# Kernel optimization log

Hardware: AMD Instinct MI355X
Metric: run time of the kernel (lower is better)

Reference implementation:

```python
import jax, jax.numpy as jnp
import numpy as np

D = 128  # d_pair
N = 512  # n_res
B = 1
EPS = 1e-5


def setup_inputs() -> dict:
    key = jax.random.key(0)
    ks = jax.random.split(key, 16)
    s = 0.02
    inp = {
        "pair": jax.random.normal(ks[0], (B, N, N, D), dtype=jnp.float32),
        "pair_mask": jnp.ones((B, N, N), dtype=jnp.float32),
        "ln_g": jnp.ones((D,), dtype=jnp.float32),
        "ln_b": jnp.zeros((D,), dtype=jnp.float32),
        "w_lp": jax.random.normal(ks[1], (D, D), dtype=jnp.float32) * s,
        "b_lp": jnp.zeros((D,), dtype=jnp.float32),
        "w_lg": jax.random.normal(ks[2], (D, D), dtype=jnp.float32) * s,
        "b_lg": jnp.zeros((D,), dtype=jnp.float32),
        "w_rp": jax.random.normal(ks[3], (D, D), dtype=jnp.float32) * s,
        "b_rp": jnp.zeros((D,), dtype=jnp.float32),
        "w_rg": jax.random.normal(ks[4], (D, D), dtype=jnp.float32) * s,
        "b_rg": jnp.zeros((D,), dtype=jnp.float32),
        "w_g": jax.random.normal(ks[5], (D, D), dtype=jnp.float32) * s,
        "b_g": jnp.zeros((D,), dtype=jnp.float32),
        "w_o": jax.random.normal(ks[6], (D, D), dtype=jnp.float32) * s,
        "b_o": jnp.zeros((D,), dtype=jnp.float32),
    }
    return inp


def _layer_norm(x, g, b):
    mu = jnp.mean(x, axis=-1, keepdims=True)
    var = jnp.mean(jnp.square(x - mu), axis=-1, keepdims=True)
    return (x - mu) * jax.lax.rsqrt(var + EPS) * g + b


def reference(pair, pair_mask, ln_g, ln_b, w_lp, b_lp, w_lg, b_lg,
              w_rp, b_rp, w_rg, b_rg, w_g, b_g, w_o, b_o):
    # [B,N,N,D] pair representation; outgoing triangle multiplication
    x = _layer_norm(pair, ln_g, ln_b)
    mask = pair_mask[..., None]  # [B,N,N,1]
    left = (x @ w_lp + b_lp) * jax.nn.sigmoid(x @ w_lg + b_lg) * mask
    right = (x @ w_rp + b_rp) * jax.nn.sigmoid(x @ w_rg + b_rg) * mask
    # outgoing: contract over j -> per-channel NxN matmul
    out = jnp.einsum('bijd,bjkd->bikd', left, right)
    out = out * jax.nn.sigmoid(x @ w_g + b_g)
    out = out @ w_o + b_o
    return out
```

## Files before the change

kernel.cpp:

```cpp
#include <hip/hip_runtime.h>

#define NN 512
#define DD 128
#define PP (NN*NN)

typedef __attribute__((ext_vector_type(8))) short short8;
typedef __attribute__((ext_vector_type(4))) float floatx4;
typedef __attribute__((ext_vector_type(4))) unsigned int uintx4;
typedef __attribute__((ext_vector_type(2))) unsigned int uintx2;

__device__ __forceinline__ unsigned short f2bf(float f) {
  unsigned int u = __float_as_uint(f);
  u += 0x7fffu + ((u >> 16) & 1u);
  return (unsigned short)(u >> 16);
}
__device__ __forceinline__ float bf2f(unsigned short h) {
  return __uint_as_float(((unsigned int)h) << 16);
}
__device__ __forceinline__ unsigned int pkbf2(float lo, float hi) {
  unsigned int r;
  asm("v_cvt_pk_bf16_f32 %0, %1, %2" : "=v"(r) : "v"(lo), "v"(hi));
  return r;
}
__device__ __forceinline__ float sigm(float x) {
  return 1.f / (1.f + __expf(-x));
}

__device__ __forceinline__ void gload_lds16(const unsigned short* g, unsigned short* l) {
  __builtin_amdgcn_global_load_lds(
      (const __attribute__((address_space(1))) unsigned int*)g,
      (__attribute__((address_space(3))) unsigned int*)l, 16, 0, 0);
}

__global__ void k0_prep(const float* __restrict__ wlp, const float* __restrict__ wlg,
                        const float* __restrict__ wrp, const float* __restrict__ wrg,
                        const float* __restrict__ wg,  const float* __restrict__ wo,
                        unsigned short* __restrict__ wt) {
  const float* src[6] = {wlp, wlg, wrp, wrg, wg, wo};
  int m = blockIdx.y;
  int idx = blockIdx.x * 256 + threadIdx.x;
  int d = idx >> 7, e = idx & 127;
  wt[m * 16384 + e * 128 + d] = f2bf(src[m][d * 128 + e]);
}

__launch_bounds__(256, 8)
__global__ void k1a_ln(const float* __restrict__ pair,
                       const float* __restrict__ lng, const float* __restrict__ lnb,
                       unsigned short* __restrict__ xln) {
  const int t = threadIdx.x;
  const int sub = t & 31;
  const long row0 = (long)blockIdx.x * 128 + (t >> 5);
  const floatx4 g4 = *(const floatx4*)(lng + sub * 4);
  const floatx4 b4 = *(const floatx4*)(lnb + sub * 4);
  const float* src = pair + row0 * DD + sub * 4;
  unsigned short* dst = xln + row0 * DD + sub * 4;
  floatx4 vn = *(const floatx4*)src;
  #pragma unroll
  for (int pass = 0; pass < 16; ++pass) {
    floatx4 v = vn;
    if (pass < 15) vn = *(const floatx4*)(src + (pass + 1) * 8 * DD);
    float s  = v.x + v.y + v.z + v.w;
    float s2 = v.x * v.x + v.y * v.y + v.z * v.z + v.w * v.w;
    #pragma unroll
    for (int m = 1; m < 32; m <<= 1) {
      s  += __shfl_xor(s, m);
      s2 += __shfl_xor(s2, m);
    }
    float mu = s * (1.f / 128.f);
    float rs = rsqrtf(s2 * (1.f / 128.f) - mu * mu + 1e-5f);
    uintx2 o;
    o[0] = pkbf2((v.x - mu) * rs * g4.x + b4.x, (v.y - mu) * rs * g4.y + b4.y);
    o[1] = pkbf2((v.z - mu) * rs * g4.z + b4.z, (v.w - mu) * rs * g4.w + b4.w);
    *(uintx2*)(dst + pass * 8 * DD) = o;
  }
}

__launch_bounds__(512, 4)
__global__ void k1b_proj(const unsigned short* __restrict__ xln,
                         const float* __restrict__ pmask,
                         const unsigned short* __restrict__ wt,
                         const float* __restrict__ b_lp, const float* __restrict__ b_lg,
                         const float* __restrict__ b_rp, const float* __restrict__ b_rg,
                         const float* __restrict__ b_g,
                         unsigned short* __restrict__ left_t,
                         unsigned short* __restrict__ right_bt,
                         unsigned short* __restrict__ gate_t) {
  __shared__ __align__(16) unsigned short Sm[24576];
  __shared__ float Mlds[128];

  const int t = threadIdx.x;
  const int unit = blockIdx.y;
  const int q = blockIdx.x;

  int j0 = 0, kk = 0;
  long p0 = 0, soff;
  if (unit == 1) {
    j0 = (q >> 9) << 7; kk = q & 511;
    soff = (long)kk * NN + j0;
  } else {
    p0 = (long)q << 7;
    soff = p0;
  }
  auto arow = [&](int r) -> long {
    return (unit == 1) ? ((long)(j0 + r) * NN + kk) : (p0 + r);
  };

  if (unit < 2 && t < 128) Mlds[t] = pmask[arow(t)];

  const unsigned short* wA = wt + (unit == 0 ? 0 : unit == 1 ? 2 : 4) * 16384;
  const unsigned short* wB = wt + (unit == 0 ? 1 : 3) * 16384;

  const int lane = t & 63, w = t >> 6;
  const int ln = lane & 15, q8 = lane >> 4;
  const int wm = (w >> 2) << 6, we = (w & 3) << 5;
  const int sr = t >> 2, sc = t & 3;

  const long aBase = arow(sr) * DD + sc * 8;

  auto STAGE = [&](int set, int kc) {
    unsigned short* base = Sm + set * 12288;
    gload_lds16(xln + aBase + kc * 32,            &base[t * 8]);
    gload_lds16(wA + sr * 128 + kc * 32 + sc * 8, &base[4096 + t * 8]);
    if (unit < 2)
      gload_lds16(wB + sr * 128 + kc * 32 + sc * 8, &base[8192 + t * 8]);
  };

  floatx4 aP[4][2] = {}, aG[4][2] = {};
  STAGE(0, 0);
  __syncthreads();
  #pragma unroll
  for (int kc = 0; kc < 4; ++kc) {
    const int cur = kc & 1;
    if (kc < 3) STAGE(cur ^ 1, kc + 1);
    unsigned short* Al = Sm + cur * 12288;
    unsigned short* Bp = Al + 4096;
    unsigned short* Bg = Al + 8192;
    short8 a[4];
    #pragma unroll
    for (int i = 0; i < 4; ++i)
      a[i] = *(const short8*)&Al[(wm + i * 16 + ln) * 32 + q8 * 8];
    #pragma unroll
    for (int j = 0; j < 2; ++j) {
      short8 bpv = *(const short8*)&Bp[(we + j * 16 + ln) * 32 + q8 * 8];
      #pragma unroll
      for (int i = 0; i < 4; ++i)
        aP[i][j] = __builtin_amdgcn_mfma_f32_16x16x32_bf16(a[i], bpv, aP[i][j], 0, 0, 0);
    }
    if (unit < 2) {
      #pragma unroll
      for (int j = 0; j < 2; ++j) {
        short8 bgv = *(const short8*)&Bg[(we + j * 16 + ln) * 32 + q8 * 8];
        #pragma unroll
        for (int i = 0; i < 4; ++i)
          aG[i][j] = __builtin_amdgcn_mfma_f32_16x16x32_bf16(a[i], bgv, aG[i][j], 0, 0, 0);
      }
    }
    __syncthreads();
  }

  unsigned short* mystg = Sm + w * 2176;
  if (unit < 2) {
    const float* bpp = (unit == 0) ? b_lp : b_rp;
    const float* bgg = (unit == 0) ? b_lg : b_rg;
    #pragma unroll
    for (int j = 0; j < 2; ++j) {
      int eg = we + j * 16 + ln;
      float bp = bpp[eg], bg = bgg[eg];
      #pragma unroll
      for (int i = 0; i < 4; ++i) {
        float vv[4];
        #pragma unroll
        for (int r = 0; r < 4; ++r) {
          int m = wm + i * 16 + q8 * 4 + r;
          vv[r] = (aP[i][j][r] + bp) * sigm(aG[i][j][r] + bg) * Mlds[m];
        }
        unsigned int* du = (unsigned int*)&mystg[(j * 16 + ln) * 68 + i * 16 + q8 * 4];
        du[0] = pkbf2(vv[0], vv[1]);
        du[1] = pkbf2(vv[2], vv[3]);
      }
    }
  } else {
    #pragma unroll
    for (int j = 0; j < 2; ++j) {
      int eg = we + j * 16 + ln;
      float bg = b_g[eg];
      #pragma unroll
      for (int i = 0; i < 4; ++i) {
        float vv[4];
        #pragma unroll
        for (int r = 0; r < 4; ++r)
          vv[r] = sigm(aP[i][j][r] + bg);
        unsigned int* du = (unsigned int*)&mystg[(j * 16 + ln) * 68 + i * 16 + q8 * 4];
        du[0] = pkbf2(vv[0], vv[1]);
        du[1] = pkbf2(vv[2], vv[3]);
      }
    }
  }

  unsigned short* dstbase = (unit == 0) ? left_t : (unit == 1 ? right_bt : gate_t);
  #pragma unroll
  for (int itr = 0; itr < 4; ++itr) {
    int row = itr * 8 + (lane >> 3);
    int c = lane & 7;
    short8 vv = *(const short8*)&mystg[row * 68 + c * 8];
    long eg = we + row;
    *(short8*)(dstbase + eg * PP + soff + wm + c * 8) = vv;
  }
}

__launch_bounds__(512, 4)
__global__ void k2_einsum(const unsigned short* __restrict__ left_t,
                          const unsigned short* __restrict__ right_bt,
                          const unsigned short* __restrict__ gate_t,
                          unsigned short* __restrict__ tmpg) {
  __shared__ __align__(16) unsigned short Sm[16896];
  unsigned short* Cl = Sm;
  const int t = threadIdx.x;
  const int h = blockIdx.x;
  const int L = (h & 7) * 256 + (h >> 3);
  const int d = L >> 4;
  const int tile = L & 15;
  const int i0 = (tile >> 2) << 7;
  const int k0 = (tile & 3) << 7;
  const unsigned short* Ag = left_t   + (long)d * PP;
  const unsigned short* Bg = right_bt + (long)d * PP;
  const unsigned short* Gg = gate_t   + (long)d * PP;
  const int lane = t & 63, w = t >> 6;
  const int ln = lane & 15, q8 = lane >> 4;
  const int wm = (w >> 2) << 6, wn = (w & 3) << 5;
  const int sr = t >> 2, sc = t & 3;

  const long aBase = (long)(i0 + sr) * NN + sc * 8;
  const long bBase = (long)(k0 + sr) * NN + sc * 8;

  auto STAGE = [&](int set, int jj) {
    gload_lds16(Ag + aBase + jj, &Sm[set * 8192 + t * 8]);
    gload_lds16(Bg + bBase + jj, &Sm[set * 8192 + 4096 + t * 8]);
  };

  floatx4 acc[4][2] = {};
  STAGE(0, 0);
  __syncthreads();
  for (int it = 0; it < 16; ++it) {
    const int cur = it & 1;
    if (it < 15) STAGE(cur ^ 1, (it + 1) * 32);
    unsigned short* Al = Sm + cur * 8192;
    unsigned short* Bl = Al + 4096;
    short8 a[4], b[2];
    #pragma unroll
    for (int i = 0; i < 4; ++i)
      a[i] = *(const short8*)&Al[(wm + i * 16 + ln) * 32 + q8 * 8];
    #pragma unroll
    for (int j = 0; j < 2; ++j)
      b[j] = *(const short8*)&Bl[(wn + j * 16 + ln) * 32 + q8 * 8];
    #pragma unroll
    for (int i = 0; i < 4; ++i)
      #pragma unroll
      for (int j = 0; j < 2; ++j)
        acc[i][j] = __builtin_amdgcn_mfma_f32_16x16x32_bf16(a[i], b[j], acc[i][j], 0, 0, 0);
    __syncthreads();
  }
  #pragma unroll
  for (int i = 0; i < 4; ++i)
    #pragma unroll
    for (int j = 0; j < 2; ++j) {
      int n = wn + j * 16 + ln;
      #pragma unroll
      for (int r = 0; r < 4; ++r) {
        int m = wm + i * 16 + q8 * 4 + r;
        float gf = bf2f(Gg[(long)(i0 + m) * NN + k0 + n]);
        Cl[m * 132 + n] = f2bf(acc[i][j][r] * gf);
      }
    }
  __syncthreads();
  unsigned short* Og = tmpg + (long)d * PP;
  #pragma unroll
  for (int it = 0; it < 4; ++it) {
    int flat = it * 512 + t;
    int m = flat >> 4, c = flat & 15;
    *(short8*)(Og + (long)(i0 + m) * NN + k0 + c * 8) = *(const short8*)&Cl[m * 132 + c * 8];
  }
}

__launch_bounds__(512, 4)
__global__ void k3_out(const unsigned short* __restrict__ tmpg,
                       const unsigned short* __restrict__ wt,
                       const float* __restrict__ b_o,
                       float* __restrict__ out) {
  __shared__ __align__(16) unsigned short Tl[128 * 144];
  unsigned int* TlU = (unsigned int*)Tl;
  const int t = threadIdx.x;
  const long p0 = (long)blockIdx.x << 7;
  const unsigned short* wo = wt + 5 * 16384;

  #pragma unroll
  for (int it = 0; it < 2; ++it) {
    int flat = it * 512 + t;
    int rp = flat >> 4;
    int c  = flat & 15;
    const unsigned short* ra = tmpg + (long)(2 * rp) * PP + p0 + c * 8;
    uintx4 xa = *(const uintx4*)ra;
    uintx4 xb = *(const uintx4*)(ra + PP);
    int sw = ((c & 7) << 3) ^ ((c >> 3) << 2);
    #pragma unroll
    for (int cc = 0; cc < 4; ++cc) {
      int p = c * 8 + 2 * cc;
      TlU[p * 72 + (rp ^ sw)]       = (xa[cc] & 0xffffu) | (xb[cc] << 16);
      TlU[(p + 1) * 72 + (rp ^ sw)] = (xa[cc] >> 16) | (xb[cc] & 0xffff0000u);
    }
  }
  __syncthreads();

  const int lane = t & 63, w = t >> 6;
  const int ln = lane & 15, q8 = lane >> 4;
  const int wm = (w >> 2) << 6, wn = (w & 3) << 5;

  floatx4 acc[4][2] = {};
  #pragma unroll
  for (int ks = 0; ks < 4; ++ks) {
    short8 a[4], b[2];
    #pragma unroll
    for (int i = 0; i < 4; ++i) {
      int p = wm + i * 16 + ln;
      int swh = (((p >> 3) & 7) << 4) ^ (((p >> 6) & 1) << 3);
      a[i] = *(const short8*)&Tl[p * 144 + ((ks * 32 + q8 * 8) ^ swh)];
    }
    #pragma unroll
    for (int j = 0; j < 2; ++j)
      b[j] = *(const short8*)(wo + (wn + j * 16 + ln) * 128 + ks * 32 + q8 * 8);
    #pragma unroll
    for (int i = 0; i < 4; ++i)
      #pragma unroll
      for (int j = 0; j < 2; ++j)
        acc[i][j] = __builtin_amdgcn_mfma_f32_16x16x32_bf16(a[i], b[j], acc[i][j], 0, 0, 0);
  }
  #pragma unroll
  for (int j = 0; j < 2; ++j) {
    int eg = wn + j * 16 + ln;
    float bias = b_o[eg];
    #pragma unroll
    for (int i = 0; i < 4; ++i)
      #pragma unroll
      for (int r = 0; r < 4; ++r) {
        int m = wm + i * 16 + q8 * 4 + r;
        out[(p0 + m) * DD + eg] = acc[i][j][r] + bias;
      }
  }
}

extern "C" void kernel_launch(void* const* d_in, const int* in_sizes, int n_in,
                              void* d_out, int out_size, void* d_ws, size_t ws_size,
                              hipStream_t stream) {
  const float* pair = (const float*)d_in[0];
  const float* pmask = (const float*)d_in[1];
  const float* ln_g = (const float*)d_in[2];
  const float* ln_b = (const float*)d_in[3];
  const float* w_lp = (const float*)d_in[4];
  const float* b_lp = (const float*)d_in[5];
  const float* w_lg = (const float*)d_in[6];
  const float* b_lg = (const float*)d_in[7];
  const float* w_rp = (const float*)d_in[8];
  const float* b_rp = (const float*)d_in[9];
  const float* w_rg = (const float*)d_in[10];
  const float* b_rg = (const float*)d_in[11];
  const float* w_g  = (const float*)d_in[12];
  const float* b_g  = (const float*)d_in[13];
  const float* w_o  = (const float*)d_in[14];
  const float* b_o  = (const float*)d_in[15];
  float* out = (float*)d_out;

  char* ws = (char*)d_ws;
  unsigned short* wt       = (unsigned short*)ws;
  unsigned short* xln      = (unsigned short*)(ws + 196608);
  unsigned short* left_t   = xln      + (size_t)PP * DD;
  unsigned short* right_bt = left_t   + (size_t)PP * DD;
  unsigned short* gate_t   = right_bt + (size_t)PP * DD;
  unsigned short* tmpg     = xln;

  k0_prep<<<dim3(64, 6), 256, 0, stream>>>(w_lp, w_lg, w_rp, w_rg, w_g, w_o, wt);
  k1a_ln<<<dim3(2048), 256, 0, stream>>>(pair, ln_g, ln_b, xln);
  k1b_proj<<<dim3(2048, 3), 512, 0, stream>>>(xln, pmask, wt,
      b_lp, b_lg, b_rp, b_rg, b_g, left_t, right_bt, gate_t);
  k2_einsum<<<dim3(2048), 512, 0, stream>>>(left_t, right_bt, gate_t, tmpg);
  k3_out<<<dim3(2048), 512, 0, stream>>>(tmpg, wt, b_o, out);
}
```

Baseline: 477.1 us.

## Split projection kernel so left and gate share one staged xln tile

The single three-unit projection kernel becomes two kernels. One computes both the gate and the left projections from one 128-row xln tile kept in LDS across all four k-chunks. The other computes the right projection with its transposed row access. This removes one of the three global reads of the xln tile per row block. In exchange the combined kernel uses more LDS (about 70KB), which may lower occupancy, and its weight loads are no longer double-buffered, so loads and MFMA work overlap less.

Result: slower. 491.2 us (+3.0%).

```diff
diff --git a/kernel.cpp b/kernel.cpp
--- a/kernel.cpp
+++ b/kernel.cpp
@@ -76,53 +76,169 @@
 }
 
 __launch_bounds__(512, 4)
-__global__ void k1b_proj(const unsigned short* __restrict__ xln,
-                         const float* __restrict__ pmask,
-                         const unsigned short* __restrict__ wt,
-                         const float* __restrict__ b_lp, const float* __restrict__ b_lg,
-                         const float* __restrict__ b_rp, const float* __restrict__ b_rg,
-                         const float* __restrict__ b_g,
-                         unsigned short* __restrict__ left_t,
-                         unsigned short* __restrict__ right_bt,
-                         unsigned short* __restrict__ gate_t) {
-  __shared__ __align__(16) unsigned short Sm[24576];
+__global__ void k1b_lg(const unsigned short* __restrict__ xln,
+                       const float* __restrict__ pmask,
+                       const unsigned short* __restrict__ wt,
+                       const float* __restrict__ b_lp, const float* __restrict__ b_lg,
+                       const float* __restrict__ b_g,
+                       unsigned short* __restrict__ left_t,
+                       unsigned short* __restrict__ gate_t) {
+  __shared__ __align__(16) unsigned short Sm[34816];
   __shared__ float Mlds[128];
+  unsigned short* Areg = Sm;
+  unsigned short* Wreg = Sm + 17408;
 
   const int t = threadIdx.x;
-  const int unit = blockIdx.y;
-  const int q = blockIdx.x;
-
-  int j0 = 0, kk = 0;
-  long p0 = 0, soff;
-  if (unit == 1) {
-    j0 = (q >> 9) << 7; kk = q & 511;
-    soff = (long)kk * NN + j0;
-  } else {
-    p0 = (long)q << 7;
-    soff = p0;
-  }
-  auto arow = [&](int r) -> long {
-    return (unit == 1) ? ((long)(j0 + r) * NN + kk) : (p0 + r);
-  };
-
-  if (unit < 2 && t < 128) Mlds[t] = pmask[arow(t)];
-
-  const unsigned short* wA = wt + (unit == 0 ? 0 : unit == 1 ? 2 : 4) * 16384;
-  const unsigned short* wB = wt + (unit == 0 ? 1 : 3) * 16384;
+  const long p0 = (long)blockIdx.x << 7;
+  if (t < 128) Mlds[t] = pmask[p0 + t];
 
   const int lane = t & 63, w = t >> 6;
   const int ln = lane & 15, q8 = lane >> 4;
   const int wm = (w >> 2) << 6, we = (w & 3) << 5;
   const int sr = t >> 2, sc = t & 3;
 
+  const unsigned short* wlp = wt;
+  const unsigned short* wlg = wt + 16384;
+  const unsigned short* wg  = wt + 4 * 16384;
+
+  #pragma unroll
+  for (int kc = 0; kc < 4; ++kc)
+    gload_lds16(xln + (p0 + sr) * DD + kc * 32 + sc * 8, &Areg[kc * 4096 + t * 8]);
+
+  floatx4 aG2[4][2] = {};
+  #pragma unroll
+  for (int kc = 0; kc < 4; ++kc) {
+    gload_lds16(wg + sr * 128 + kc * 32 + sc * 8, &Wreg[t * 8]);
+    __syncthreads();
+    short8 a[4];
+    #pragma unroll
+    for (int i = 0; i < 4; ++i)
+      a[i] = *(const short8*)&Areg[kc * 4096 + (wm + i * 16 + ln) * 32 + q8 * 8];
+    #pragma unroll
+    for (int j = 0; j < 2; ++j) {
+      short8 bv = *(const short8*)&Wreg[(we + j * 16 + ln) * 32 + q8 * 8];
+      #pragma unroll
+      for (int i = 0; i < 4; ++i)
+        aG2[i][j] = __builtin_amdgcn_mfma_f32_16x16x32_bf16(a[i], bv, aG2[i][j], 0, 0, 0);
+    }
+    __syncthreads();
+  }
+  {
+    unsigned short* stg = Wreg + w * 2176;
+    #pragma unroll
+    for (int j = 0; j < 2; ++j) {
+      int eg = we + j * 16 + ln;
+      float bg = b_g[eg];
+      #pragma unroll
+      for (int i = 0; i < 4; ++i) {
+        float vv[4];
+        #pragma unroll
+        for (int r = 0; r < 4; ++r)
+          vv[r] = sigm(aG2[i][j][r] + bg);
+        unsigned int* du = (unsigned int*)&stg[(j * 16 + ln) * 68 + i * 16 + q8 * 4];
+        du[0] = pkbf2(vv[0], vv[1]);
+        du[1] = pkbf2(vv[2], vv[3]);
+      }
+    }
+    #pragma unroll
+    for (int itr = 0; itr < 4; ++itr) {
+      int row = itr * 8 + (lane >> 3);
+      int c = lane & 7;
+      short8 vv = *(const short8*)&stg[row * 68 + c * 8];
+      long eg = we + row;
+      *(short8*)(gate_t + eg * PP + p0 + wm + c * 8) = vv;
+    }
+  }
+  __syncthreads();
+
+  floatx4 aP[4][2] = {}, aG[4][2] = {};
+  #pragma unroll
+  for (int kc = 0; kc < 4; ++kc) {
+    gload_lds16(wlp + sr * 128 + kc * 32 + sc * 8, &Wreg[t * 8]);
+    gload_lds16(wlg + sr * 128 + kc * 32 + sc * 8, &Wreg[4096 + t * 8]);
+    __syncthreads();
+    short8 a[4];
+    #pragma unroll
+    for (int i = 0; i < 4; ++i)
+      a[i] = *(const short8*)&Areg[kc * 4096 + (wm + i * 16 + ln) * 32 + q8 * 8];
+    #pragma unroll
+    for (int j = 0; j < 2; ++j) {
+      short8 bpv = *(const short8*)&Wreg[(we + j * 16 + ln) * 32 + q8 * 8];
+      #pragma unroll
+      for (int i = 0; i < 4; ++i)
+        aP[i][j] = __builtin_amdgcn_mfma_f32_16x16x32_bf16(a[i], bpv, aP[i][j], 0, 0, 0);
+    }
+    #pragma unroll
+    for (int j = 0; j < 2; ++j) {
+      short8 bgv = *(const short8*)&Wreg[4096 + (we + j * 16 + ln) * 32 + q8 * 8];
+      #pragma unroll
+      for (int i = 0; i < 4; ++i)
+        aG[i][j] = __builtin_amdgcn_mfma_f32_16x16x32_bf16(a[i], bgv, aG[i][j], 0, 0, 0);
+    }
+    __syncthreads();
+  }
+  {
+    unsigned short* stg = Areg + w * 2176;
+    #pragma unroll
+    for (int j = 0; j < 2; ++j) {
+      int eg = we + j * 16 + ln;
+      float bp = b_lp[eg], bg = b_lg[eg];
+      #pragma unroll
+      for (int i = 0; i < 4; ++i) {
+        float vv[4];
+        #pragma unroll
+        for (int r = 0; r < 4; ++r) {
+          int m = wm + i * 16 + q8 * 4 + r;
+          vv[r] = (aP[i][j][r] + bp) * sigm(aG[i][j][r] + bg) * Mlds[m];
+        }
+        unsigned int* du = (unsigned int*)&stg[(j * 16 + ln) * 68 + i * 16 + q8 * 4];
+        du[0] = pkbf2(vv[0], vv[1]);
+        du[1] = pkbf2(vv[2], vv[3]);
+      }
+    }
+    #pragma unroll
+    for (int itr = 0; itr < 4; ++itr) {
+      int row = itr * 8 + (lane >> 3);
+      int c = lane & 7;
+      short8 vv = *(const short8*)&stg[row * 68 + c * 8];
+      long eg = we + row;
+      *(short8*)(left_t + eg * PP + p0 + wm + c * 8) = vv;
+    }
+  }
+}
+
+__launch_bounds__(512, 4)
+__global__ void k1b_r(const unsigned short* __restrict__ xln,
+                      const float* __restrict__ pmask,
+                      const unsigned short* __restrict__ wt,
+                      const float* __restrict__ b_rp, const float* __restrict__ b_rg,
+                      unsigned short* __restrict__ right_bt) {
+  __shared__ __align__(16) unsigned short Sm[24576];
+  __shared__ float Mlds[128];
+
+  const int t = threadIdx.x;
+  const int q = blockIdx.x;
+  const int j0 = (q >> 9) << 7, kk = q & 511;
+  const long soff = (long)kk * NN + j0;
+  auto arow = [&](int r) -> long { return (long)(j0 + r) * NN + kk; };
+
+  if (t < 128) Mlds[t] = pmask[arow(t)];
+
+  const unsigned short* wA = wt + 2 * 16384;
+  const unsigned short* wB = wt + 3 * 16384;
+
+  const int lane = t & 63, w = t >> 6;
+  const int ln = lane & 15, q8 = lane >> 4;
+  const int wm = (w >> 2) << 6, we = (w & 3) << 5;
+  const int sr = t >> 2, sc = t & 3;
+
   const long aBase = arow(sr) * DD + sc * 8;
 
   auto STAGE = [&](int set, int kc) {
     unsigned short* base = Sm + set * 12288;
     gload_lds16(xln + aBase + kc * 32,            &base[t * 8]);
     gload_lds16(wA + sr * 128 + kc * 32 + sc * 8, &base[4096 + t * 8]);
-    if (unit < 2)
-      gload_lds16(wB + sr * 128 + kc * 32 + sc * 8, &base[8192 + t * 8]);
+    gload_lds16(wB + sr * 128 + kc * 32 + sc * 8, &base[8192 + t * 8]);
   };
 
   floatx4 aP[4][2] = {}, aG[4][2] = {};
@@ -146,65 +262,41 @@
       for (int i = 0; i < 4; ++i)
         aP[i][j] = __builtin_amdgcn_mfma_f32_16x16x32_bf16(a[i], bpv, aP[i][j], 0, 0, 0);
     }
-    if (unit < 2) {
-      #pragma unroll
-      for (int j = 0; j < 2; ++j) {
-        short8 bgv = *(const short8*)&Bg[(we + j * 16 + ln) * 32 + q8 * 8];
-        #pragma unroll
-        for (int i = 0; i < 4; ++i)
-          aG[i][j] = __builtin_amdgcn_mfma_f32_16x16x32_bf16(a[i], bgv, aG[i][j], 0, 0, 0);
+    #pragma unroll
+    for (int j = 0; j < 2; ++j) {
+      short8 bgv = *(const short8*)&Bg[(we + j * 16 + ln) * 32 + q8 * 8];
+      #pragma unroll
+      for (int i = 0; i < 4; ++i)
+        aG[i][j] = __builtin_amdgcn_mfma_f32_16x16x32_bf16(a[i], bgv, aG[i][j], 0, 0, 0);
+    }
+    __syncthreads();
+  }
+
+  unsigned short* mystg = Sm + w * 2176;
+  #pragma unroll
+  for (int j = 0; j < 2; ++j) {
+    int eg = we + j * 16 + ln;
+    float bp = b_rp[eg], bg = b_rg[eg];
+    #pragma unroll
+    for (int i = 0; i < 4; ++i) {
+      float vv[4];
+      #pragma unroll
+      for (int r = 0; r < 4; ++r) {
+        int m = wm + i * 16 + q8 * 4 + r;
+        vv[r] = (aP[i][j][r] + bp) * sigm(aG[i][j][r] + bg) * Mlds[m];
       }
-    }
-    __syncthreads();
-  }
-
-  unsigned short* mystg = Sm + w * 2176;
-  if (unit < 2) {
-    const float* bpp = (unit == 0) ? b_lp : b_rp;
-    const float* bgg = (unit == 0) ? b_lg : b_rg;
-    #pragma unroll
-    for (int j = 0; j < 2; ++j) {
-      int eg = we + j * 16 + ln;
-      float bp = bpp[eg], bg = bgg[eg];
-      #pragma unroll
-      for (int i = 0; i < 4; ++i) {
-        float vv[4];
-        #pragma unroll
-        for (int r = 0; r < 4; ++r) {
-          int m = wm + i * 16 + q8 * 4 + r;
-          vv[r] = (aP[i][j][r] + bp) * sigm(aG[i][j][r] + bg) * Mlds[m];
-        }
-        unsigned int* du = (unsigned int*)&mystg[(j * 16 + ln) * 68 + i * 16 + q8 * 4];
-        du[0] = pkbf2(vv[0], vv[1]);
-        du[1] = pkbf2(vv[2], vv[3]);
-      }
-    }
-  } else {
-    #pragma unroll
-    for (int j = 0; j < 2; ++j) {
-      int eg = we + j * 16 + ln;
-      float bg = b_g[eg];
-      #pragma unroll
-      for (int i = 0; i < 4; ++i) {
-        float vv[4];
-        #pragma unroll
-        for (int r = 0; r < 4; ++r)
-          vv[r] = sigm(aP[i][j][r] + bg);
-        unsigned int* du = (unsigned int*)&mystg[(j * 16 + ln) * 68 + i * 16 + q8 * 4];
-        du[0] = pkbf2(vv[0], vv[1]);
-        du[1] = pkbf2(vv[2], vv[3]);
-      }
-    }
-  }
-
-  unsigned short* dstbase = (unit == 0) ? left_t : (unit == 1 ? right_bt : gate_t);
+      unsigned int* du = (unsigned int*)&mystg[(j * 16 + ln) * 68 + i * 16 + q8 * 4];
+      du[0] = pkbf2(vv[0], vv[1]);
+      du[1] = pkbf2(vv[2], vv[3]);
+    }
+  }
   #pragma unroll
   for (int itr = 0; itr < 4; ++itr) {
     int row = itr * 8 + (lane >> 3);
     int c = lane & 7;
     short8 vv = *(const short8*)&mystg[row * 68 + c * 8];
     long eg = we + row;
-    *(short8*)(dstbase + eg * PP + soff + wm + c * 8) = vv;
+    *(short8*)(right_bt + eg * PP + soff + wm + c * 8) = vv;
   }
 }
 
@@ -379,8 +471,9 @@
 
   k0_prep<<<dim3(64, 6), 256, 0, stream>>>(w_lp, w_lg, w_rp, w_rg, w_g, w_o, wt);
   k1a_ln<<<dim3(2048), 256, 0, stream>>>(pair, ln_g, ln_b, xln);
-  k1b_proj<<<dim3(2048, 3), 512, 0, stream>>>(xln, pmask, wt,
-      b_lp, b_lg, b_rp, b_rg, b_g, left_t, right_bt, gate_t);
+  k1b_lg<<<dim3(2048), 512, 0, stream>>>(xln, pmask, wt, b_lp, b_lg, b_g,
+                                         left_t, gate_t);
+  k1b_r<<<dim3(2048), 512, 0, stream>>>(xln, pmask, wt, b_rp, b_rg, right_bt);
   k2_einsum<<<dim3(2048), 512, 0, stream>>>(left_t, right_bt, gate_t, tmpg);
   k3_out<<<dim3(2048), 512, 0, stream>>>(tmpg, wt, b_o, out);
 }
```
